# Optimization experiments

Measured on AMD Instinct MI355X. Metric: run time of the kernel, lower is better.

## Reference

```python
import jax, jax.numpy as jnp
import numpy as np

DET_COUNT = 729
N_ANGLES = 90
IMG = 512
FEATURES = 32
FILTER_SIZE = max(64, int(2 ** np.ceil(np.log2(2 * DET_COUNT))))  # 2048


def _ramp_filter(size):
    # scikit-image / torch_radon style spatial-domain ram-lak, then FFT
    n = np.concatenate([np.arange(1, size // 2 + 1, 2), np.arange(size // 2 - 1, 0, -2)])
    f = np.zeros(size, dtype=np.float64)
    f[0] = 0.25
    f[1::2] = -1.0 / (np.pi * n) ** 2
    return jnp.asarray(2.0 * np.real(np.fft.fft(f)), dtype=jnp.float32)

_RAMP = _ramp_filter(FILTER_SIZE)


def radon_forward(img, theta, det_count):
    # parallel-beam line integrals; img: (B, C, n, n)
    B, C, n, _ = img.shape
    c = (n - 1) / 2.0
    s = jnp.arange(det_count, dtype=img.dtype) - (det_count - 1) / 2.0  # detector offsets == ray steps
    cos, sin = jnp.cos(theta), jnp.sin(theta)
    # sample points: p = c + s*dir_perp + t*dir_ray   -> coords (A, D, T)
    px = c + s[None, :, None] * cos[:, None, None] - s[None, None, :] * sin[:, None, None]
    py = c + s[None, :, None] * sin[:, None, None] + s[None, None, :] * cos[:, None, None]

    def sample(im2d):
        vals = jax.scipy.ndimage.map_coordinates(im2d, [py, px], order=1, mode='constant', cval=0.0)
        return vals.sum(-1)  # integrate along ray -> (A, D)

    sino = jax.vmap(sample)(img.reshape(B * C, n, n))
    return sino.reshape(B, C, theta.shape[0], det_count)


def filter_sinogram(sino, n_angles):
    det = sino.shape[-1]
    padded = jnp.pad(sino, ((0, 0), (0, 0), (0, 0), (0, FILTER_SIZE - det)))
    out = jnp.real(jnp.fft.ifft(jnp.fft.fft(padded, axis=-1) * _RAMP, axis=-1))[..., :det]
    return out * (jnp.pi / (2.0 * n_angles))


def radon_backprojection(sino, theta, n):
    B, C, A, D = sino.shape
    c = (n - 1) / 2.0
    xs = jnp.arange(n, dtype=sino.dtype) - c
    X = xs[None, :]  # columns -> x
    Y = xs[:, None]  # rows    -> y
    cos, sin = jnp.cos(theta), jnp.sin(theta)
    pos = X[None] * cos[:, None, None] + Y[None] * sin[:, None, None] + (D - 1) / 2.0  # (A, n, n)
    i0 = jnp.clip(jnp.floor(pos), 0, D - 2).astype(jnp.int32)
    w = pos - i0
    valid = (pos >= 0) & (pos <= D - 1)

    def back_one(sino_ad):  # (A, D) -> (n, n)
        def per_angle(row, idx, ww, vv):
            v = row[idx] * (1.0 - ww) + row[idx + 1] * ww
            return jnp.where(vv, v, 0.0)
        return jax.vmap(per_angle)(sino_ad, i0, w, valid).sum(0)

    return jax.vmap(back_one)(sino.reshape(B * C, A, D)).reshape(B, C, n, n)


def conv2d(x, w):
    return jax.lax.conv_general_dilated(x, w, (1, 1), 'SAME', dimension_numbers=('NCHW', 'OIHW', 'NCHW'))


def setup_inputs():
    key = jax.random.key(0)
    ks = jax.random.split(key, 10)

    def xavier(k, shape):
        fan_in = shape[1] * shape[2] * shape[3]
        fan_out = shape[0] * shape[2] * shape[3]
        std = float(np.sqrt(2.0 / (fan_in + fan_out)))
        return jax.random.normal(k, shape, dtype=jnp.float32) * std

    x = jax.random.normal(ks[0], (1, 1, IMG, IMG), dtype=jnp.float32)
    theta = jnp.linspace(0.0, np.pi, N_ANGLES, endpoint=False).astype(jnp.float32)
    sinogram = jax.random.normal(ks[1], (1, 1, N_ANGLES, DET_COUNT), dtype=jnp.float32)
    return {
        'x': x, 'theta': theta, 'sinogram': sinogram,
        'lambda_step': jnp.asarray([0.5], dtype=jnp.float32),
        'soft_thr': jnp.asarray([0.01], dtype=jnp.float32),
        'conv_D': xavier(ks[2], (FEATURES, 1, 3, 3)),
        'conv1_forward': xavier(ks[3], (FEATURES, FEATURES, 3, 3)),
        'conv2_forward': xavier(ks[4], (FEATURES, FEATURES, 3, 3)),
        'conv1_backward': xavier(ks[5], (FEATURES, FEATURES, 3, 3)),
        'conv2_backward': xavier(ks[6], (FEATURES, FEATURES, 3, 3)),
        'conv_G': xavier(ks[7], (1, FEATURES, 3, 3)),
    }


def reference(x, theta, sinogram, lambda_step, soft_thr, conv_D, conv1_forward, conv2_forward, conv1_backward, conv2_backward, conv_G):
    sino_pred = radon_forward(x, theta, DET_COUNT)
    filtered = filter_sinogram(sino_pred, theta.shape[0])
    X_fbp = radon_backprojection(filtered - sinogram, theta, x.shape[2])
    x_input = x - lambda_step[0] * X_fbp

    x_D = conv2d(x_input, conv_D)
    h = jax.nn.relu(conv2d(x_D, conv1_forward))
    x_forward = conv2d(h, conv2_forward)
    st = jnp.sign(x_forward) * jax.nn.relu(jnp.abs(x_forward) - soft_thr[0])
    h = jax.nn.relu(conv2d(st, conv1_backward))
    x_backward = conv2d(h, conv2_backward)
    x_G = conv2d(x_backward, conv_G)
    x_pred = x_input + x_G

    h = jax.nn.relu(conv2d(x_forward, conv1_backward))
    x_D_est = conv2d(h, conv2_backward)
    symloss = x_D_est - x_D
    return (x_pred, symloss, symloss)
```

## Files before the change

### kernel.cpp

```cpp
#include <hip/hip_runtime.h>

#define IMG   512
#define NA    90
#define DET   729
#define NPIX  (IMG*IMG)
#define HW    514
#define QW    514
#define HBELEMS (HW*HW*32)

typedef __attribute__((ext_vector_type(8))) short     bf16x8;
typedef __attribute__((ext_vector_type(8))) unsigned short ushort8;
typedef __attribute__((ext_vector_type(4))) float     f32x4;

__device__ __forceinline__ unsigned short f2b(float f) {
    unsigned int u = __builtin_bit_cast(unsigned int, f);
    return (unsigned short)((u + 0x7FFFu + ((u >> 16) & 1u)) >> 16);
}
__device__ __forceinline__ float b2f(unsigned short h) {
    return __builtin_bit_cast(float, (unsigned int)h << 16);
}

__global__ void prep0_k(const float* __restrict__ theta, const float* __restrict__ img,
                        float* __restrict__ trig, uint2* __restrict__ quad) {
    if (blockIdx.x == 0) {
        int i = threadIdx.x;
        if (i < NA) {
            float t = theta[i];
            trig[2*i]   = cosf(t);
            trig[2*i+1] = sinf(t);
        }
        return;
    }
    int q = (blockIdx.x - 1) * 256 + threadIdx.x;
    if (q >= QW*QW) return;
    int qy = q / QW, qx = q - qy*QW;
    auto val = [&](int r, int c) -> float {
        return (r >= 1 && r <= 512 && c >= 1 && c <= 512) ? img[((r-1) << 9) + (c-1)] : 0.f;
    };
    unsigned int lo = (unsigned int)f2b(val(qy, qx))   | ((unsigned int)f2b(val(qy, qx+1))   << 16);
    unsigned int hi = (unsigned int)f2b(val(qy+1, qx)) | ((unsigned int)f2b(val(qy+1, qx+1)) << 16);
    quad[q] = make_uint2(lo, hi);
}

__global__ __launch_bounds__(256) void radon_fwd_k(const uint2* __restrict__ quad,
        const float* __restrict__ trig, float* __restrict__ sino) {
    int wid  = threadIdx.x >> 6;
    int lane = threadIdx.x & 63;
    int idx  = blockIdx.x * 4 + wid;
    if (idx >= NA*DET) return;
    int a = idx / DET, d = idx - a*DET;
    float cs = trig[2*a], sn = trig[2*a+1];
    float sd = (float)d - 364.0f;
    float bx = 255.5f + sd*cs;
    float by = 255.5f + sd*sn;

    float inv_sn = 1.0f / sn;
    float ta = (bx - 512.0f) * inv_sn, tb = (bx + 1.0f) * inv_sn;
    float lo = fminf(ta, tb), hi = fmaxf(ta, tb);
    float inv_cs = 1.0f / cs;
    float tc = (-1.0f - by) * inv_cs, td = (512.0f - by) * inv_cs;
    lo = fmaxf(lo, fminf(tc, td));
    hi = fminf(hi, fmaxf(tc, td));
    float jlo_f = fminf(fmaxf(lo + 364.0f, 0.0f), 729.0f);
    float jhi_f = fminf(fmaxf(hi + 364.0f, -1.0f), 728.0f);
    int jlo = (int)ceilf(jlo_f);
    int jhi = (int)floorf(jhi_f);

    auto samp = [&](float pxr, float pyr) -> float {
        float cx = fminf(fmaxf(pxr, -1.0f), 512.0f);
        float cy = fminf(fmaxf(pyr, -1.0f), 512.0f);
        float fx0 = floorf(cx), fy0 = floorf(cy);
        float fx = cx - fx0, fy = cy - fy0;
        int qi = (int)fy0 * QW + (int)fx0 + (QW + 1);
        uint2 q = quad[qi];
        float v00 = __builtin_bit_cast(float, q.x << 16);
        float v01 = __builtin_bit_cast(float, q.x & 0xffff0000u);
        float v10 = __builtin_bit_cast(float, q.y << 16);
        float v11 = __builtin_bit_cast(float, q.y & 0xffff0000u);
        float top = v00 + fx*(v01 - v00);
        float bot = v10 + fx*(v11 - v10);
        return top + fy*(bot - top);
    };

    float acc = 0.f;
    int j = jlo + lane;
    float s0 = (float)(j - 364);
    float px1 = bx - s0*sn,          py1 = by + s0*cs;
    float px2 = px1 - 64.0f*sn,      py2 = py1 + 64.0f*cs;
    float dx128 = -128.0f*sn,        dy128 = 128.0f*cs;
    for (; j + 64 <= jhi; j += 128) {
        acc += samp(px1, py1) + samp(px2, py2);
        px1 += dx128; py1 += dy128;
        px2 += dx128; py2 += dy128;
    }
    if (j <= jhi) acc += samp(px1, py1);

    for (int off = 32; off; off >>= 1) acc += __shfl_down(acc, off);
    if (lane == 0) sino[idx] = acc;
}

__global__ __launch_bounds__(256) void filter_k(const float* __restrict__ sino,
        const float* __restrict__ meas, float* __restrict__ diff) {
    __shared__ float prow[DET + 2*728];
    __shared__ float invsq[364];
    int a = blockIdx.x / 3, seg = blockIdx.x - 3*a;
    for (int t = threadIdx.x; t < DET + 2*728; t += 256)
        prow[t] = (t >= 728 && t < 728 + DET) ? sino[a*DET + (t - 728)] : 0.f;
    const float cc = -2.0f / (3.14159265358979323846f * 3.14159265358979323846f);
    for (int k = threadIdx.x; k < 364; k += 256) {
        float dlt = (float)(2*k + 1);
        invsq[k] = cc / (dlt * dlt);
    }
    __syncthreads();
    const float scale = 3.14159265358979323846f / 180.0f;
    int i = seg*243 + threadIdx.x;
    if (threadIdx.x < 243) {
        const float* p = prow + 728 + i;
        float acc = 0.5f * p[0];
        #pragma unroll 4
        for (int k = 0; k < 364; k++) {
            int dlt = 2*k + 1;
            acc += (p[-dlt] + p[dlt]) * invsq[k];
        }
        diff[a*DET + i] = acc * scale - meas[a*DET + i];
    }
}

__global__ void pair_k(const float* __restrict__ diff, float2* __restrict__ pair) {
    int i = blockIdx.x * 256 + threadIdx.x;
    if (i >= NA*DET) return;
    int col = i - (i / DET) * DET;
    float b = (col == DET-1) ? 0.f : diff[i + 1];
    pair[i] = make_float2(diff[i], b);
}

__global__ __launch_bounds__(256) void backproj_k(const float2* __restrict__ pair,
        const float* __restrict__ trig, const float* __restrict__ x,
        const float* __restrict__ lam, float* __restrict__ xin) {
    int pix = blockIdx.x * 256 + threadIdx.x;
    float X = (float)(pix & 511) - 255.5f;
    float Y = (float)(pix >> 9) - 255.5f;
    float acc = 0.f;
    for (int a = 0; a < NA; a++) {
        float pos = X*trig[2*a] + Y*trig[2*a+1] + 364.0f;
        if (pos >= 0.f && pos <= 728.f) {
            int i0 = (int)pos;
            if (i0 > 727) i0 = 727;
            float w = pos - (float)i0;
            float2 p = pair[a*DET + i0];
            acc += p.x + w*(p.y - p.x);
        }
    }
    xin[pix] = x[pix] - lam[0] * acc;
}

__global__ void prep1_k(unsigned short* __restrict__ hb0, size_t hbstride_elems,
                        const float* __restrict__ w0, const float* __restrict__ w1,
                        const float* __restrict__ w2, const float* __restrict__ w3,
                        const float* __restrict__ wg4,
                        unsigned short* __restrict__ wbuf) {
    int t = blockIdx.x * 256 + threadIdx.x;
    if (t < 4*2052) {
        int b = t / 2052, r = t - b*2052;
        int py, px;
        if      (r < 514)  { py = 0;            px = r; }
        else if (r < 1028) { py = 513;          px = r - 514; }
        else if (r < 1540) { py = r - 1028 + 1; px = 0; }
        else               { py = r - 1540 + 1; px = 513; }
        unsigned short* p = hb0 + b*hbstride_elems + ((size_t)py*HW + px)*32;
        uint4 z = make_uint4(0,0,0,0);
        ((uint4*)p)[0] = z; ((uint4*)p)[1] = z; ((uint4*)p)[2] = z; ((uint4*)p)[3] = z;
        return;
    }
    int tid = t - 4*2052;
    if (tid < 4*9216) {
        int L = tid / 9216, r = tid - L*9216;
        int tt = r >> 10, o = (r >> 5) & 31, i = r & 31;
        const float* s = (L == 0) ? w0 : (L == 1) ? w1 : (L == 2) ? w2 : w3;
        wbuf[tid] = f2b(s[o*288 + i*9 + tt]);
        return;
    }
    int gid = tid - 4*9216;
    if (gid >= 9*512) return;
    int tt = gid / 512, r = gid - tt*512;
    int o = r >> 5, i = r & 31;
    wbuf[4*9216 + gid] = (o == 0) ? f2b(wg4[i*9 + tt]) : (unsigned short)0;
}

__global__ __launch_bounds__(256) void convD_k(const float* __restrict__ xin,
        const float* __restrict__ wD, unsigned short* __restrict__ out_nhwc) {
    int pix = blockIdx.x * 256 + threadIdx.x;
    int y = pix >> 9, x = pix & 511;
    float v[9];
    #pragma unroll
    for (int dy = -1; dy <= 1; dy++)
        #pragma unroll
        for (int dx = -1; dx <= 1; dx++) {
            int yy = y + dy, xx = x + dx;
            v[(dy+1)*3 + dx+1] = (yy >= 0 && yy < 512 && xx >= 0 && xx < 512)
                                 ? xin[(yy << 9) + xx] : 0.f;
        }
    unsigned int packed[16];
    #pragma unroll
    for (int oc = 0; oc < 32; ++oc) {
        float acc = 0.f;
        #pragma unroll
        for (int t = 0; t < 9; t++) acc = fmaf(v[t], wD[oc*9 + t], acc);
        unsigned int b = f2b(acc);
        if (oc & 1) packed[oc >> 1] |= b << 16; else packed[oc >> 1] = b;
    }
    uint4* dst = (uint4*)(out_nhwc + ((size_t)(y+1)*HW + (x+1))*32);
    dst[0] = make_uint4(packed[0],  packed[1],  packed[2],  packed[3]);
    dst[1] = make_uint4(packed[4],  packed[5],  packed[6],  packed[7]);
    dst[2] = make_uint4(packed[8],  packed[9],  packed[10], packed[11]);
    dst[3] = make_uint4(packed[12], packed[13], packed[14], packed[15]);
}

template<int MODE>
__global__ __launch_bounds__(256) void convM_k(const unsigned short* __restrict__ in,
        const unsigned short* __restrict__ wb,
        unsigned short* __restrict__ out0, unsigned short* __restrict__ out1,
        const float* __restrict__ thr_p,
        const unsigned short* __restrict__ aux, float* __restrict__ s1, float* __restrict__ s2) {
    int wid  = threadIdx.x >> 6;
    int lane = threadIdx.x & 63;
    int by = blockIdx.x >> 3, bx = blockIdx.x & 7;
    int y  = by*4 + wid;
    int x0 = bx*64;
    int lpix = lane & 15;
    int k8   = (lane >> 4) * 8;

    bf16x8 A[9][2];
    #pragma unroll
    for (int t = 0; t < 9; t++)
        #pragma unroll
        for (int ob = 0; ob < 2; ob++)
            A[t][ob] = *(const bf16x8*)(wb + t*1024 + (ob*16 + lpix)*32 + k8);

    f32x4 acc[2][4];
    #pragma unroll
    for (int ob = 0; ob < 2; ob++)
        #pragma unroll
        for (int p = 0; p < 4; p++) acc[ob][p] = (f32x4){0.f,0.f,0.f,0.f};

    const short* base = (const short*)in + ((size_t)(y+1)*HW + (x0+1) + lpix)*32 + k8;
    #pragma unroll
    for (int dy = -1; dy <= 1; dy++)
        #pragma unroll
        for (int dx = -1; dx <= 1; dx++) {
            int t = (dy+1)*3 + (dx+1);
            const short* bp = base + (dy*HW + dx)*32;
            #pragma unroll
            for (int p = 0; p < 4; p++) {
                bf16x8 B = *(const bf16x8*)(bp + p*16*32);
                acc[0][p] = __builtin_amdgcn_mfma_f32_16x16x32_bf16(A[t][0], B, acc[0][p], 0,0,0);
                acc[1][p] = __builtin_amdgcn_mfma_f32_16x16x32_bf16(A[t][1], B, acc[1][p], 0,0,0);
            }
        }

    int prow = (lane >> 4) * 4;
    float thr = (MODE == 2) ? thr_p[0] : 0.f;
    #pragma unroll
    for (int ob = 0; ob < 2; ob++)
        #pragma unroll
        for (int p = 0; p < 4; p++) {
            f32x4 a = acc[ob][p];
            if (MODE == 3) {
                size_t aoff = ((size_t)(y+1)*HW + (x0 + 1 + p*16 + lpix))*32 + ob*16 + prow;
                ushort4 av = *(const ushort4*)(aux + aoff);
                int pix = (y << 9) + x0 + p*16 + lpix;
                float w0v = a[0] - b2f(av.x);
                float w1v = a[1] - b2f(av.y);
                float w2v = a[2] - b2f(av.z);
                float w3v = a[3] - b2f(av.w);
                int ocb = ob*16 + prow;
                s1[(size_t)(ocb+0)*NPIX + pix] = w0v; s2[(size_t)(ocb+0)*NPIX + pix] = w0v;
                s1[(size_t)(ocb+1)*NPIX + pix] = w1v; s2[(size_t)(ocb+1)*NPIX + pix] = w1v;
                s1[(size_t)(ocb+2)*NPIX + pix] = w2v; s2[(size_t)(ocb+2)*NPIX + pix] = w2v;
                s1[(size_t)(ocb+3)*NPIX + pix] = w3v; s2[(size_t)(ocb+3)*NPIX + pix] = w3v;
            } else {
                size_t off = ((size_t)(y+1)*HW + (x0 + 1 + p*16 + lpix))*32 + ob*16 + prow;
                if (MODE == 1) {
                    #pragma unroll
                    for (int r = 0; r < 4; r++) a[r] = fmaxf(a[r], 0.f);
                }
                *(ushort4*)(out0 + off) = make_ushort4(f2b(a[0]), f2b(a[1]), f2b(a[2]), f2b(a[3]));
                if (MODE == 2) {
                    float st[4];
                    #pragma unroll
                    for (int r = 0; r < 4; r++)
                        st[r] = copysignf(fmaxf(fabsf(a[r]) - thr, 0.f), a[r]);
                    *(ushort4*)(out1 + off) = make_ushort4(f2b(st[0]), f2b(st[1]), f2b(st[2]), f2b(st[3]));
                }
            }
        }
}

__global__ __launch_bounds__(256) void convGM_k(const unsigned short* __restrict__ in,
        const unsigned short* __restrict__ wg,
        const float* __restrict__ xin, float* __restrict__ out) {
    int wid  = threadIdx.x >> 6;
    int lane = threadIdx.x & 63;
    int by = blockIdx.x >> 3, bx = blockIdx.x & 7;
    int y  = by*4 + wid;
    int x0 = bx*64;
    int lpix = lane & 15;
    int k8   = (lane >> 4) * 8;

    bf16x8 A[9];
    #pragma unroll
    for (int t = 0; t < 9; t++)
        A[t] = *(const bf16x8*)(wg + t*512 + lpix*32 + k8);

    f32x4 acc[4];
    #pragma unroll
    for (int p = 0; p < 4; p++) acc[p] = (f32x4){0.f,0.f,0.f,0.f};

    const short* base = (const short*)in + ((size_t)(y+1)*HW + (x0+1) + lpix)*32 + k8;
    #pragma unroll
    for (int dy = -1; dy <= 1; dy++)
        #pragma unroll
        for (int dx = -1; dx <= 1; dx++) {
            int t = (dy+1)*3 + (dx+1);
            const short* bp = base + (dy*HW + dx)*32;
            #pragma unroll
            for (int p = 0; p < 4; p++) {
                bf16x8 B = *(const bf16x8*)(bp + p*16*32);
                acc[p] = __builtin_amdgcn_mfma_f32_16x16x32_bf16(A[t], B, acc[p], 0,0,0);
            }
        }

    if (lane < 16) {
        #pragma unroll
        for (int p = 0; p < 4; p++) {
            int pix = (y << 9) + x0 + p*16 + lane;
            out[pix] = acc[p][0] + xin[pix];
        }
    }
}

extern "C" void kernel_launch(void* const* d_in, const int* in_sizes, int n_in,
                              void* d_out, int out_size, void* d_ws, size_t ws_size,
                              hipStream_t stream) {
    const float* x     = (const float*)d_in[0];
    const float* theta = (const float*)d_in[1];
    const float* meas  = (const float*)d_in[2];
    const float* lam   = (const float*)d_in[3];
    const float* thr   = (const float*)d_in[4];
    const float* wD    = (const float*)d_in[5];
    const float* w1f   = (const float*)d_in[6];
    const float* w2f   = (const float*)d_in[7];
    const float* w1b   = (const float*)d_in[8];
    const float* w2b   = (const float*)d_in[9];
    const float* wG    = (const float*)d_in[10];

    char* ws = (char*)d_ws;
    const size_t HBB = (size_t)HBELEMS * 2;
    unsigned short* HB1 = (unsigned short*)(ws);
    unsigned short* HB2 = (unsigned short*)(ws + HBB);
    unsigned short* HB3 = (unsigned short*)(ws + 2*HBB);
    unsigned short* HB4 = (unsigned short*)(ws + 3*HBB);
    float*  sino  = (float*)(ws + HBB);
    float*  diff  = (float*)(ws + HBB + 262464);
    float2* dpair = (float2*)(ws + HBB + 524928);
    uint2*  quad  = (uint2*)(ws + 2*HBB);
    float* xin  = (float*)(ws + 4*HBB);
    float* trig = (float*)(ws + 4*HBB + 1048576);
    unsigned short* wbuf = (unsigned short*)(ws + 4*HBB + 1049600);
    unsigned short* wgbuf = wbuf + 4*9216;

    float* P  = (float*)d_out;
    float* S1 = P + NPIX;
    float* S2 = S1 + 32*NPIX;

    prep0_k<<<1 + (QW*QW + 255)/256, 256, 0, stream>>>(theta, x, trig, quad);
    radon_fwd_k<<<(NA*DET + 3)/4, 256, 0, stream>>>(quad, trig, sino);
    filter_k<<<NA*3, 256, 0, stream>>>(sino, meas, diff);
    pair_k<<<(NA*DET + 255)/256, 256, 0, stream>>>(diff, dpair);
    backproj_k<<<NPIX/256, 256, 0, stream>>>(dpair, trig, x, lam, xin);
    prep1_k<<<(4*2052 + 4*9216 + 9*512 + 255)/256, 256, 0, stream>>>(HB1, HBELEMS,
                                             w1f, w2f, w1b, w2b, wG, wbuf);

    convD_k<<<NPIX/256, 256, 0, stream>>>(xin, wD, HB1);
    convM_k<1><<<1024, 256, 0, stream>>>(HB1, wbuf + 0*9216, HB2, nullptr,
                                         nullptr, nullptr, nullptr, nullptr);
    convM_k<2><<<1024, 256, 0, stream>>>(HB2, wbuf + 1*9216, HB3, HB4,
                                         thr, nullptr, nullptr, nullptr);
    convM_k<1><<<1024, 256, 0, stream>>>(HB4, wbuf + 2*9216, HB2, nullptr,
                                         nullptr, nullptr, nullptr, nullptr);
    convM_k<0><<<1024, 256, 0, stream>>>(HB2, wbuf + 3*9216, HB4, nullptr,
                                         nullptr, nullptr, nullptr, nullptr);
    convGM_k<<<1024, 256, 0, stream>>>(HB4, wgbuf, xin, P);
    convM_k<1><<<1024, 256, 0, stream>>>(HB3, wbuf + 2*9216, HB2, nullptr,
                                         nullptr, nullptr, nullptr, nullptr);
    convM_k<3><<<1024, 256, 0, stream>>>(HB2, wbuf + 3*9216, nullptr, nullptr,
                                         nullptr, HB1, S1, S2);
}
```

Measured before the change: 232.2 us.

## Tile radon forward projection through LDS and restructure conv row reuse

Replaces the per-ray forward projector with a tiled kernel: each block stages a 32x32 tile of the bilinear quad image in shared memory, walks the rays of 30 angles that cross the tile, and accumulates partial line integrals into a zeroed sinogram with atomics. Separately, the MFMA 3x3 conv kernel now covers 16-wide by 4-row output patches per wave and loads each input row once, reusing it across up to three output rows. The aim is less global gather traffic for the projector and fewer redundant input loads in the convs. The cost is many atomics with a serial per-lane ray walk, and a float summation order that differs from before.

```diff
diff --git a/kernel.cpp b/kernel.cpp
--- a/kernel.cpp
+++ b/kernel.cpp
@@ -21,7 +21,8 @@
 }
 
 __global__ void prep0_k(const float* __restrict__ theta, const float* __restrict__ img,
-                        float* __restrict__ trig, uint2* __restrict__ quad) {
+                        float* __restrict__ trig, uint2* __restrict__ quad,
+                        float* __restrict__ sino) {
     if (blockIdx.x == 0) {
         int i = threadIdx.x;
         if (i < NA) {
@@ -31,72 +32,98 @@
         }
         return;
     }
-    int q = (blockIdx.x - 1) * 256 + threadIdx.x;
-    if (q >= QW*QW) return;
-    int qy = q / QW, qx = q - qy*QW;
-    auto val = [&](int r, int c) -> float {
-        return (r >= 1 && r <= 512 && c >= 1 && c <= 512) ? img[((r-1) << 9) + (c-1)] : 0.f;
-    };
-    unsigned int lo = (unsigned int)f2b(val(qy, qx))   | ((unsigned int)f2b(val(qy, qx+1))   << 16);
-    unsigned int hi = (unsigned int)f2b(val(qy+1, qx)) | ((unsigned int)f2b(val(qy+1, qx+1)) << 16);
-    quad[q] = make_uint2(lo, hi);
-}
-
-__global__ __launch_bounds__(256) void radon_fwd_k(const uint2* __restrict__ quad,
+    if (blockIdx.x <= 1033) {
+        int q = (blockIdx.x - 1) * 256 + threadIdx.x;
+        if (q >= QW*QW) return;
+        int qy = q / QW, qx = q - qy*QW;
+        auto val = [&](int r, int c) -> float {
+            return (r >= 1 && r <= 512 && c >= 1 && c <= 512) ? img[((r-1) << 9) + (c-1)] : 0.f;
+        };
+        unsigned int lo = (unsigned int)f2b(val(qy, qx))   | ((unsigned int)f2b(val(qy, qx+1))   << 16);
+        unsigned int hi = (unsigned int)f2b(val(qy+1, qx)) | ((unsigned int)f2b(val(qy+1, qx+1)) << 16);
+        quad[q] = make_uint2(lo, hi);
+        return;
+    }
+    int z = (blockIdx.x - 1034) * 256 + threadIdx.x;
+    if (z < NA*DET) sino[z] = 0.f;
+}
+
+__global__ __launch_bounds__(256) void radon_tile_k(const uint2* __restrict__ quad,
         const float* __restrict__ trig, float* __restrict__ sino) {
-    int wid  = threadIdx.x >> 6;
-    int lane = threadIdx.x & 63;
-    int idx  = blockIdx.x * 4 + wid;
-    if (idx >= NA*DET) return;
-    int a = idx / DET, d = idx - a*DET;
-    float cs = trig[2*a], sn = trig[2*a+1];
-    float sd = (float)d - 364.0f;
-    float bx = 255.5f + sd*cs;
-    float by = 255.5f + sd*sn;
-
-    float inv_sn = 1.0f / sn;
-    float ta = (bx - 512.0f) * inv_sn, tb = (bx + 1.0f) * inv_sn;
-    float lo = fminf(ta, tb), hi = fmaxf(ta, tb);
-    float inv_cs = 1.0f / cs;
-    float tc = (-1.0f - by) * inv_cs, td = (512.0f - by) * inv_cs;
-    lo = fmaxf(lo, fminf(tc, td));
-    hi = fminf(hi, fmaxf(tc, td));
-    float jlo_f = fminf(fmaxf(lo + 364.0f, 0.0f), 729.0f);
-    float jhi_f = fminf(fmaxf(hi + 364.0f, -1.0f), 728.0f);
-    int jlo = (int)ceilf(jlo_f);
-    int jhi = (int)floorf(jhi_f);
-
-    auto samp = [&](float pxr, float pyr) -> float {
-        float cx = fminf(fmaxf(pxr, -1.0f), 512.0f);
-        float cy = fminf(fmaxf(pyr, -1.0f), 512.0f);
-        float fx0 = floorf(cx), fy0 = floorf(cy);
-        float fx = cx - fx0, fy = cy - fy0;
-        int qi = (int)fy0 * QW + (int)fx0 + (QW + 1);
-        uint2 q = quad[qi];
-        float v00 = __builtin_bit_cast(float, q.x << 16);
-        float v01 = __builtin_bit_cast(float, q.x & 0xffff0000u);
-        float v10 = __builtin_bit_cast(float, q.y << 16);
-        float v11 = __builtin_bit_cast(float, q.y & 0xffff0000u);
-        float top = v00 + fx*(v01 - v00);
-        float bot = v10 + fx*(v11 - v10);
-        return top + fy*(bot - top);
-    };
-
-    float acc = 0.f;
-    int j = jlo + lane;
-    float s0 = (float)(j - 364);
-    float px1 = bx - s0*sn,          py1 = by + s0*cs;
-    float px2 = px1 - 64.0f*sn,      py2 = py1 + 64.0f*cs;
-    float dx128 = -128.0f*sn,        dy128 = 128.0f*cs;
-    for (; j + 64 <= jhi; j += 128) {
-        acc += samp(px1, py1) + samp(px2, py2);
-        px1 += dx128; py1 += dy128;
-        px2 += dx128; py2 += dy128;
-    }
-    if (j <= jhi) acc += samp(px1, py1);
-
-    for (int off = 32; off; off >>= 1) acc += __shfl_down(acc, off);
-    if (lane == 0) sino[idx] = acc;
+    __shared__ uint2 tl[32*33];
+    __shared__ float strig[60];
+    int b  = blockIdx.x;
+    int ag = b % 3;
+    int tq = b / 3;
+    int tx = tq % 17, ty = tq / 17;
+    int X0 = tx*32, Y0 = ty*32;
+    int tid = threadIdx.x;
+
+    for (int i = tid; i < 32*32; i += 256) {
+        int qy = i >> 5, qx = i & 31;
+        int gx = X0 + qx, gy = Y0 + qy;
+        uint2 v = make_uint2(0u, 0u);
+        if (gx < QW && gy < QW) v = quad[gy*QW + gx];
+        tl[qy*33 + qx] = v;
+    }
+    if (tid < 60) strig[tid] = trig[60*ag + tid];
+    __syncthreads();
+
+    float fX0 = (float)X0 - 1.0f;
+    float fY0 = (float)Y0 - 1.0f;
+    int w = tid >> 6, lane = tid & 63;
+
+    for (int g = 0; g < 8; ++g) {
+        int asub = w + 4*g;
+        if (asub >= 30) break;
+        float cs = strig[2*asub], sn = strig[2*asub+1];
+        int a = 30*ag + asub;
+        float cx0 = fX0 - 255.5f, cx1 = cx0 + 32.0f;
+        float cy0 = fY0 - 255.5f, cy1 = cy0 + 32.0f;
+        float sdmin = fminf(cx0*cs, cx1*cs) + fminf(cy0*sn, cy1*sn);
+        float sdmax = fmaxf(cx0*cs, cx1*cs) + fmaxf(cy0*sn, cy1*sn);
+        int dmin = (int)ceilf(sdmin + 364.0f) - 1; if (dmin < 0) dmin = 0;
+        int dmax = (int)floorf(sdmax + 364.0f) + 1; if (dmax > DET-1) dmax = DET-1;
+        int d = dmin + lane;
+        if (d > dmax) continue;
+        float sd = (float)d - 364.0f;
+        float bx = 255.5f + sd*cs, by = 255.5f + sd*sn;
+        float lo = -365.0f, hi = 365.0f;
+        if (sn > 1e-7f) {
+            float inv = 1.0f / sn;
+            lo = (bx - (fX0 + 32.0f)) * inv;
+            hi = (bx - fX0) * inv;
+        } else if (bx < fX0 || bx >= fX0 + 32.0f) continue;
+        if (fabsf(cs) > 1e-7f) {
+            float inv = 1.0f / cs;
+            float s1 = (fY0 - by) * inv, s2 = (fY0 + 32.0f - by) * inv;
+            lo = fmaxf(lo, fminf(s1, s2));
+            hi = fminf(hi, fmaxf(s1, s2));
+        } else if (by < fY0 || by >= fY0 + 32.0f) continue;
+        int jlo = (int)ceilf(lo + 364.0f) - 1; if (jlo < 0) jlo = 0;
+        int jhi = (int)floorf(hi + 364.0f) + 1; if (jhi > DET-1) jhi = DET-1;
+        if (jlo > jhi) continue;
+        float sj = (float)jlo - 364.0f;
+        float px = bx - sj*sn - fX0;
+        float py = by + sj*cs - fY0;
+        float acc = 0.f;
+        for (int j = jlo; j <= jhi; ++j) {
+            if (px >= 0.f && px < 32.f && py >= 0.f && py < 32.f) {
+                int ix = (int)px, iy = (int)py;
+                float fx = px - (float)ix, fy = py - (float)iy;
+                uint2 q = tl[iy*33 + ix];
+                float v00 = __builtin_bit_cast(float, q.x << 16);
+                float v01 = __builtin_bit_cast(float, q.x & 0xffff0000u);
+                float v10 = __builtin_bit_cast(float, q.y << 16);
+                float v11 = __builtin_bit_cast(float, q.y & 0xffff0000u);
+                float top = v00 + fx*(v01 - v00);
+                float bot = v10 + fx*(v11 - v10);
+                acc += top + fy*(bot - top);
+            }
+            px -= sn; py += cs;
+        }
+        if (acc != 0.f) atomicAdd(&sino[a*DET + d], acc);
+    }
 }
 
 __global__ __launch_bounds__(256) void filter_k(const float* __restrict__ sino,
@@ -222,11 +249,11 @@
         unsigned short* __restrict__ out0, unsigned short* __restrict__ out1,
         const float* __restrict__ thr_p,
         const unsigned short* __restrict__ aux, float* __restrict__ s1, float* __restrict__ s2) {
-    int wid  = threadIdx.x >> 6;
+    int wv   = threadIdx.x >> 6;
     int lane = threadIdx.x & 63;
-    int by = blockIdx.x >> 3, bx = blockIdx.x & 7;
-    int y  = by*4 + wid;
-    int x0 = bx*64;
+    int bx = blockIdx.x & 31, by = blockIdx.x >> 5;
+    int x0 = bx*16;
+    int yb = by*16 + wv*4;
     int lpix = lane & 15;
     int k8   = (lane >> 4) * 8;
 
@@ -241,34 +268,37 @@
     #pragma unroll
     for (int ob = 0; ob < 2; ob++)
         #pragma unroll
-        for (int p = 0; p < 4; p++) acc[ob][p] = (f32x4){0.f,0.f,0.f,0.f};
-
-    const short* base = (const short*)in + ((size_t)(y+1)*HW + (x0+1) + lpix)*32 + k8;
-    #pragma unroll
-    for (int dy = -1; dy <= 1; dy++)
-        #pragma unroll
-        for (int dx = -1; dx <= 1; dx++) {
-            int t = (dy+1)*3 + (dx+1);
-            const short* bp = base + (dy*HW + dx)*32;
+        for (int o = 0; o < 4; o++) acc[ob][o] = (f32x4){0.f,0.f,0.f,0.f};
+
+    const short* base = (const short*)in + ((size_t)yb*HW + (x0 + lpix))*32 + k8;
+    #pragma unroll
+    for (int r = 0; r < 6; ++r) {
+        #pragma unroll
+        for (int dx = 0; dx < 3; ++dx) {
+            bf16x8 B = *(const bf16x8*)(base + ((size_t)r*HW + dx)*32);
             #pragma unroll
-            for (int p = 0; p < 4; p++) {
-                bf16x8 B = *(const bf16x8*)(bp + p*16*32);
-                acc[0][p] = __builtin_amdgcn_mfma_f32_16x16x32_bf16(A[t][0], B, acc[0][p], 0,0,0);
-                acc[1][p] = __builtin_amdgcn_mfma_f32_16x16x32_bf16(A[t][1], B, acc[1][p], 0,0,0);
+            for (int dy = 0; dy < 3; ++dy) {
+                int o = r - dy;
+                if (o >= 0 && o < 4) {
+                    int t = dy*3 + dx;
+                    acc[0][o] = __builtin_amdgcn_mfma_f32_16x16x32_bf16(A[t][0], B, acc[0][o], 0,0,0);
+                    acc[1][o] = __builtin_amdgcn_mfma_f32_16x16x32_bf16(A[t][1], B, acc[1][o], 0,0,0);
+                }
             }
         }
+    }
 
     int prow = (lane >> 4) * 4;
     float thr = (MODE == 2) ? thr_p[0] : 0.f;
     #pragma unroll
     for (int ob = 0; ob < 2; ob++)
         #pragma unroll
-        for (int p = 0; p < 4; p++) {
-            f32x4 a = acc[ob][p];
+        for (int o = 0; o < 4; o++) {
+            f32x4 a = acc[ob][o];
             if (MODE == 3) {
-                size_t aoff = ((size_t)(y+1)*HW + (x0 + 1 + p*16 + lpix))*32 + ob*16 + prow;
+                size_t aoff = ((size_t)(yb+o+1)*HW + (x0 + 1 + lpix))*32 + ob*16 + prow;
                 ushort4 av = *(const ushort4*)(aux + aoff);
-                int pix = (y << 9) + x0 + p*16 + lpix;
+                int pix = ((yb+o) << 9) + x0 + lpix;
                 float w0v = a[0] - b2f(av.x);
                 float w1v = a[1] - b2f(av.y);
                 float w2v = a[2] - b2f(av.z);
@@ -279,17 +309,17 @@
                 s1[(size_t)(ocb+2)*NPIX + pix] = w2v; s2[(size_t)(ocb+2)*NPIX + pix] = w2v;
                 s1[(size_t)(ocb+3)*NPIX + pix] = w3v; s2[(size_t)(ocb+3)*NPIX + pix] = w3v;
             } else {
-                size_t off = ((size_t)(y+1)*HW + (x0 + 1 + p*16 + lpix))*32 + ob*16 + prow;
+                size_t off = ((size_t)(yb+o+1)*HW + (x0 + 1 + lpix))*32 + ob*16 + prow;
                 if (MODE == 1) {
                     #pragma unroll
-                    for (int r = 0; r < 4; r++) a[r] = fmaxf(a[r], 0.f);
+                    for (int r2 = 0; r2 < 4; r2++) a[r2] = fmaxf(a[r2], 0.f);
                 }
                 *(ushort4*)(out0 + off) = make_ushort4(f2b(a[0]), f2b(a[1]), f2b(a[2]), f2b(a[3]));
                 if (MODE == 2) {
                     float st[4];
                     #pragma unroll
-                    for (int r = 0; r < 4; r++)
-                        st[r] = copysignf(fmaxf(fabsf(a[r]) - thr, 0.f), a[r]);
+                    for (int r2 = 0; r2 < 4; r2++)
+                        st[r2] = copysignf(fmaxf(fabsf(a[r2]) - thr, 0.f), a[r2]);
                     *(ushort4*)(out1 + off) = make_ushort4(f2b(st[0]), f2b(st[1]), f2b(st[2]), f2b(st[3]));
                 }
             }
@@ -373,8 +403,8 @@
     float* S1 = P + NPIX;
     float* S2 = S1 + 32*NPIX;
 
-    prep0_k<<<1 + (QW*QW + 255)/256, 256, 0, stream>>>(theta, x, trig, quad);
-    radon_fwd_k<<<(NA*DET + 3)/4, 256, 0, stream>>>(quad, trig, sino);
+    prep0_k<<<1 + 1033 + 257, 256, 0, stream>>>(theta, x, trig, quad, sino);
+    radon_tile_k<<<17*17*3, 256, 0, stream>>>(quad, trig, sino);
     filter_k<<<NA*3, 256, 0, stream>>>(sino, meas, diff);
     pair_k<<<(NA*DET + 255)/256, 256, 0, stream>>>(diff, dpair);
     backproj_k<<<NPIX/256, 256, 0, stream>>>(dpair, trig, x, lam, xin);
```

After: 247.7 us. 6.7% more time.
